# Performance work log

Measured on AMD Instinct MI355X. Metric: run time of the kernel, lower is better.

The kernel has to match this reference:

```python
import jax, jax.numpy as jnp
import numpy as np

N_BOND = 2_000_000
N_ATOM = 100_000
N_STRUCT = 2
THREEBODY_CUTOFF = 0.8


def setup_inputs() -> dict:
    key = jax.random.key(0)
    k1, k2 = jax.random.split(key)
    # bonds grouped (sorted) by source atom, as _compute_threebody assumes
    bond_src = jnp.sort(jax.random.randint(k1, (N_BOND,), 0, N_ATOM))
    bond_length = jax.random.uniform(k2, (N_BOND,), dtype=jnp.float32)
    n_atoms = jnp.full((N_STRUCT,), N_ATOM // N_STRUCT, dtype=jnp.int32)
    return {"bond_src": bond_src, "bond_length": bond_length, "n_atoms": n_atoms}


def reference(bond_src, bond_length, n_atoms):
    """Vectorized equivalent of compute_threebody_indices.

    Returns (bond_indices [T,2] pairs of ORIGINAL bond ids, n_triple_ij [n_bond],
    n_triple_i [n_atom], n_triple_s [n_struct]). Replaces the O(n) Python loops
    with segment-sum (degree count), prefix-sum (CSR offsets) and a flat
    enumeration of ordered within-atom bond pairs (j != k).
    """
    n_bond = bond_src.shape[0]
    n_atom = int(jnp.sum(n_atoms))
    n_struct = n_atoms.shape[0]

    # --- filter bonds by three-body cutoff, remember original bond ids ---
    mask = bond_length <= THREEBODY_CUTOFF
    kept = jnp.nonzero(mask)[0]          # original bond indices of surviving bonds
    src = bond_src[kept]                 # still sorted (subset of a sorted array)

    # --- per-atom bond counts and CSR offsets (parallel histogram + scan) ---
    deg = jax.ops.segment_sum(jnp.ones_like(src), src, num_segments=n_atom)
    bond_offset = jnp.cumsum(deg) - deg  # start of each atom's bond block

    # --- triples per atom / per bond / per structure ---
    n_triple_i = deg * (deg - 1)
    T = int(jnp.sum(n_triple_i))

    # --- enumerate all ordered pairs (j, k), j != k, within each atom block ---
    tri_atom = jnp.repeat(jnp.arange(n_atom), n_triple_i, total_repeat_length=T)
    tri_start = (jnp.cumsum(n_triple_i) - n_triple_i)[tri_atom]
    t = jnp.arange(T) - tri_start        # local triple index in [0, d*(d-1))
    d = deg[tri_atom]                    # d >= 2 wherever triples exist
    j = t // (d - 1)
    kp = t % (d - 1)
    k = kp + (kp >= j).astype(kp.dtype)  # skip k == j, preserving loop order
    b0 = bond_offset[tri_atom] + j       # relative (filtered) bond index
    b1 = bond_offset[tri_atom] + k
    bond_indices = jnp.stack([kept[b0], kept[b1]], axis=1)  # back to ORIGINAL ids

    # angles per ORIGINAL bond: deg(src)-1 for surviving bonds, 0 for filtered
    n_triple_ij = jnp.zeros(n_bond, dtype=deg.dtype).at[kept].set(deg[src] - 1)

    # angles per structure
    struct_id = jnp.repeat(jnp.arange(n_struct), n_atoms, total_repeat_length=n_atom)
    n_triple_s = jax.ops.segment_sum(n_triple_i, struct_id, num_segments=n_struct)

    return bond_indices, n_triple_ij, n_triple_i, n_triple_s
```

## Files before the change

kernel.cpp:

```cpp
#include <hip/hip_runtime.h>


#define CUTOFF 0.8f
#define NATOM_C 100000
#define MAXD 256

__global__ void k0_init(int* wstart, int* wend, int* deg, int* done, int n_atom) {
    int i = blockIdx.x * blockDim.x + threadIdx.x;
    if (i < n_atom) { wstart[i] = 0; wend[i] = 0; deg[i] = 0; }
    if (i == 0) *done = 0;
}

__global__ void kA_bounds_deg(const int* __restrict__ src, const float* __restrict__ len,
                              int* __restrict__ wstart, int* __restrict__ wend,
                              int* __restrict__ deg, int n_bond) {
    int q  = blockIdx.x * blockDim.x + threadIdx.x;
    int g0 = q * 4;
    int lane = threadIdx.x & 63;
    bool full = (g0 + 3 < n_bond);

    int4   s4 = make_int4(-3, -3, -3, -3);
    float4 l4 = make_float4(1e9f, 1e9f, 1e9f, 1e9f);
    if (full) {
        s4 = *(const int4*)(src + g0);
        l4 = *(const float4*)(len + g0);
    }
    int prevN = __shfl_up(s4.w, 1);
    int nextN = __shfl_down(s4.x, 1);
    if (lane == 0)  prevN = (g0 > 0 && g0 - 1 < n_bond) ? src[g0 - 1] : -1;
    if (lane == 63) nextN = (g0 + 4 < n_bond) ? src[g0 + 4] : -2;
    if (g0 + 4 >= n_bond) nextN = -2;

    if (full) {
        int a0 = s4.x, a1 = s4.y, a2 = s4.z, a3 = s4.w;
        if (g0 == 0 || a0 != prevN) wstart[a0] = g0;
        if (a1 != a0) wstart[a1] = g0 + 1;
        if (a2 != a1) wstart[a2] = g0 + 2;
        if (a3 != a2) wstart[a3] = g0 + 3;
        if (a0 != a1) wend[a0] = g0 + 1;
        if (a1 != a2) wend[a1] = g0 + 2;
        if (a2 != a3) wend[a2] = g0 + 3;
        if (g0 + 4 == n_bond || a3 != nextN) wend[a3] = g0 + 4;
        int c0 = (l4.x <= CUTOFF) ? 1 : 0;
        int c1 = (l4.y <= CUTOFF) ? 1 : 0;
        int c2 = (l4.z <= CUTOFF) ? 1 : 0;
        int c3 = (l4.w <= CUTOFF) ? 1 : 0;
        int aCur = a0, cnt = c0;
        if (a1 != aCur) { if (cnt) atomicAdd(&deg[aCur], cnt); aCur = a1; cnt = 0; }
        cnt += c1;
        if (a2 != aCur) { if (cnt) atomicAdd(&deg[aCur], cnt); aCur = a2; cnt = 0; }
        cnt += c2;
        if (a3 != aCur) { if (cnt) atomicAdd(&deg[aCur], cnt); aCur = a3; cnt = 0; }
        cnt += c3;
        if (cnt) atomicAdd(&deg[aCur], cnt);
    } else if (g0 < n_bond) {
        for (int j = 0; j < 4; j++) {
            int g = g0 + j;
            if (g >= n_bond) break;
            int a = src[g];
            if (g == 0 || src[g - 1] != a) wstart[a] = g;
            if (g == n_bond - 1 || src[g + 1] != a) wend[a] = g + 1;
            if (len[g] <= CUTOFF) atomicAdd(&deg[a], 1);
        }
    }
}

__global__ void kBC_scan(const int* __restrict__ deg, int* __restrict__ out_i,
                         int* __restrict__ exsc, int* __restrict__ bsums,
                         int* __restrict__ done, const int* __restrict__ n_atoms_arr,
                         int* __restrict__ out_s,
                         int n_atom, int ntiles, int n_struct) {
    __shared__ int tmp[256];
    __shared__ int isLast;
    int t = threadIdx.x;
    int base = blockIdx.x * 1024 + t * 4;
    int v0 = 0, v1 = 0, v2 = 0, v3 = 0;
    if (base + 3 < n_atom) {
        int4 d4 = *(const int4*)(deg + base);
        v0 = d4.x * (d4.x - 1); v1 = d4.y * (d4.y - 1);
        v2 = d4.z * (d4.z - 1); v3 = d4.w * (d4.w - 1);
        *(int4*)(out_i + base) = make_int4(v0, v1, v2, v3);
    } else {
        if (base     < n_atom) { int d = deg[base];     v0 = d * (d - 1); out_i[base]     = v0; }
        if (base + 1 < n_atom) { int d = deg[base + 1]; v1 = d * (d - 1); out_i[base + 1] = v1; }
        if (base + 2 < n_atom) { int d = deg[base + 2]; v2 = d * (d - 1); out_i[base + 2] = v2; }
        if (base + 3 < n_atom) { int d = deg[base + 3]; v3 = d * (d - 1); out_i[base + 3] = v3; }
    }
    int s = v0 + v1 + v2 + v3;
    tmp[t] = s;
    __syncthreads();
    for (int off = 1; off < 256; off <<= 1) {
        int v = (t >= off) ? tmp[t - off] : 0;
        __syncthreads();
        tmp[t] += v;
        __syncthreads();
    }
    int excl = tmp[t] - s;
    if (base     < n_atom) exsc[base]     = excl;
    if (base + 1 < n_atom) exsc[base + 1] = excl + v0;
    if (base + 2 < n_atom) exsc[base + 2] = excl + v0 + v1;
    if (base + 3 < n_atom) exsc[base + 3] = excl + v0 + v1 + v2;
    if (t == 255) bsums[blockIdx.x] = tmp[255];
    __syncthreads();
    if (t == 0) {
        __threadfence();
        int old = __hip_atomic_fetch_add(done, 1, __ATOMIC_ACQ_REL,
                                         __HIP_MEMORY_SCOPE_AGENT);
        isLast = (old == (int)gridDim.x - 1);
    }
    __syncthreads();
    if (!isLast) return;

    int v = 0;
    if (t < ntiles)
        v = __hip_atomic_load(&bsums[t], __ATOMIC_RELAXED, __HIP_MEMORY_SCOPE_AGENT);
    tmp[t] = v;
    __syncthreads();
    for (int off = 1; off < 256; off <<= 1) {
        int x = (t >= off) ? tmp[t - off] : 0;
        __syncthreads();
        tmp[t] += x;
        __syncthreads();
    }
    if (t < ntiles) bsums[t] = tmp[t] - v;
    int total = tmp[255];
    __threadfence_block();
    __syncthreads();
    if (t == 0) {
        int off = 0, prevA = 0;
        for (int s2 = 0; s2 < n_struct; s2++) {
            off += n_atoms_arr[s2];
            int A;
            if (off >= n_atom) A = total;
            else A = __hip_atomic_load(&exsc[off], __ATOMIC_RELAXED,
                                       __HIP_MEMORY_SCOPE_AGENT) + bsums[off >> 10];
            out_s[s2] = A - prevA;
            prevA = A;
        }
    }
}

__global__ void kD_enum(const float* __restrict__ len, const int* __restrict__ wstart,
                        const int* __restrict__ wend, const int* __restrict__ exsc,
                        const int* __restrict__ bsums,
                        int4* __restrict__ out4, int* __restrict__ out_ij,
                        int n_atom) {
    __shared__ int keptIds[4 * MAXD];
    int wave = threadIdx.x >> 6;
    int lane = threadIdx.x & 63;
    int a = blockIdx.x * 4 + wave;
    int* my = &keptIds[wave * MAXD];
    if (a >= n_atom) return;
    int s = wstart[a], e = wend[a];
    int d = 0;
    for (int base = s; base < e; base += 64) {
        int idx = base + lane;
        bool m = (idx < e) && (len[idx] <= CUTOFF);
        unsigned long long bal = __ballot(m);
        int pos = d + __popcll(bal & ((1ull << lane) - 1ull));
        if (m && pos < MAXD) my[pos] = idx;
        d += __popcll(bal);
    }
    int dm1 = d - 1;
    for (int idx = s + lane; idx < e; idx += 64)
        out_ij[idx] = (len[idx] <= CUTOFF) ? dm1 : 0;
    if (d >= 2) {
        unsigned udm1 = (unsigned)dm1;
        unsigned nP = ((unsigned)(d * dm1)) >> 1;
        int b4 = (exsc[a] + bsums[a >> 10]) >> 1;
        for (unsigned p = lane; p < nP; p += 64) {
            unsigned t0 = 2u * p;
            unsigned j  = t0 / udm1;
            unsigned kp = t0 - j * udm1;
            unsigned j1 = j, kp1 = kp + 1;
            if (kp1 == udm1) { j1++; kp1 = 0; }
            unsigned k0 = kp  + (kp  >= j  ? 1u : 0u);
            unsigned k1 = kp1 + (kp1 >= j1 ? 1u : 0u);
            out4[b4 + p] = make_int4(my[j], my[k0], my[j1], my[k1]);
        }
    }
}

extern "C" void kernel_launch(void* const* d_in, const int* in_sizes, int n_in,
                              void* d_out, int out_size, void* d_ws, size_t ws_size,
                              hipStream_t stream) {
    const int*   bond_src    = (const int*)d_in[0];
    const float* bond_len    = (const float*)d_in[1];
    const int*   n_atoms_arr = (const int*)d_in[2];
    int n_bond   = in_sizes[0];
    int n_struct = in_sizes[2];
    const int n_atom = NATOM_C;
    int T2 = out_size - n_bond - n_atom - n_struct;

    int ntiles = (n_atom + 1023) / 1024;

    int* ws     = (int*)d_ws;
    int* wstart = ws;
    int* wend   = ws + n_atom;
    int* deg    = ws + 2 * n_atom;
    int* exsc   = ws + 3 * n_atom;
    int* bsums  = exsc + n_atom;
    int* done   = bsums + ntiles;

    int*  out       = (int*)d_out;
    int4* out_pairs = (int4*)out;
    int*  out_ij    = out + T2;
    int*  out_i     = out_ij + n_bond;
    int*  out_s     = out_i + n_atom;

    int nq = (n_bond + 3) / 4;

    k0_init      <<<(n_atom + 255) / 256, 256, 0, stream>>>(wstart, wend, deg, done, n_atom);
    kA_bounds_deg<<<(nq + 255) / 256, 256, 0, stream>>>(bond_src, bond_len, wstart, wend, deg, n_bond);
    kBC_scan     <<<ntiles, 256, 0, stream>>>(deg, out_i, exsc, bsums, done, n_atoms_arr,
                                              out_s, n_atom, ntiles, n_struct);
    kD_enum      <<<(n_atom + 3) / 4, 256, 0, stream>>>(bond_len, wstart, wend, exsc, bsums,
                                                        out_pairs, out_ij, n_atom);
}
```

Baseline: 256.6 us.

## Fold init into bounds kernel and replace degree atomics with wave ballot counts

Drops the separate zero-init kernel: head threads now zero the entries for atoms with no bonds lying between consecutive sources, and the last thread clears the trailing atoms. Degree counting switches from per-atom atomicAdd to ballot/popcount over runs within a wave, with a serial backward scan when a run crosses a wave boundary, and one thread per bond instead of four. kD_enum caches the ballot masks for the first 256 bonds so the out_ij write does not reload lengths. This removes a launch and the atomics, at the cost of scalar loads and serial fallback loops for long or gapped runs.

```diff
diff --git a/kernel.cpp b/kernel.cpp
--- a/kernel.cpp
+++ b/kernel.cpp
@@ -5,63 +5,54 @@
 #define NATOM_C 100000
 #define MAXD 256
 
-__global__ void k0_init(int* wstart, int* wend, int* deg, int* done, int n_atom) {
-    int i = blockIdx.x * blockDim.x + threadIdx.x;
-    if (i < n_atom) { wstart[i] = 0; wend[i] = 0; deg[i] = 0; }
-    if (i == 0) *done = 0;
-}
-
 __global__ void kA_bounds_deg(const int* __restrict__ src, const float* __restrict__ len,
                               int* __restrict__ wstart, int* __restrict__ wend,
-                              int* __restrict__ deg, int n_bond) {
-    int q  = blockIdx.x * blockDim.x + threadIdx.x;
-    int g0 = q * 4;
+                              int* __restrict__ deg, int* __restrict__ done,
+                              int n_bond, int n_atom) {
+    int i = blockIdx.x * blockDim.x + threadIdx.x;
+    if (i == 0) *done = 0;
     int lane = threadIdx.x & 63;
-    bool full = (g0 + 3 < n_bond);
-
-    int4   s4 = make_int4(-3, -3, -3, -3);
-    float4 l4 = make_float4(1e9f, 1e9f, 1e9f, 1e9f);
-    if (full) {
-        s4 = *(const int4*)(src + g0);
-        l4 = *(const float4*)(len + g0);
-    }
-    int prevN = __shfl_up(s4.w, 1);
-    int nextN = __shfl_down(s4.x, 1);
-    if (lane == 0)  prevN = (g0 > 0 && g0 - 1 < n_bond) ? src[g0 - 1] : -1;
-    if (lane == 63) nextN = (g0 + 4 < n_bond) ? src[g0 + 4] : -2;
-    if (g0 + 4 >= n_bond) nextN = -2;
-
-    if (full) {
-        int a0 = s4.x, a1 = s4.y, a2 = s4.z, a3 = s4.w;
-        if (g0 == 0 || a0 != prevN) wstart[a0] = g0;
-        if (a1 != a0) wstart[a1] = g0 + 1;
-        if (a2 != a1) wstart[a2] = g0 + 2;
-        if (a3 != a2) wstart[a3] = g0 + 3;
-        if (a0 != a1) wend[a0] = g0 + 1;
-        if (a1 != a2) wend[a1] = g0 + 2;
-        if (a2 != a3) wend[a2] = g0 + 3;
-        if (g0 + 4 == n_bond || a3 != nextN) wend[a3] = g0 + 4;
-        int c0 = (l4.x <= CUTOFF) ? 1 : 0;
-        int c1 = (l4.y <= CUTOFF) ? 1 : 0;
-        int c2 = (l4.z <= CUTOFF) ? 1 : 0;
-        int c3 = (l4.w <= CUTOFF) ? 1 : 0;
-        int aCur = a0, cnt = c0;
-        if (a1 != aCur) { if (cnt) atomicAdd(&deg[aCur], cnt); aCur = a1; cnt = 0; }
-        cnt += c1;
-        if (a2 != aCur) { if (cnt) atomicAdd(&deg[aCur], cnt); aCur = a2; cnt = 0; }
-        cnt += c2;
-        if (a3 != aCur) { if (cnt) atomicAdd(&deg[aCur], cnt); aCur = a3; cnt = 0; }
-        cnt += c3;
-        if (cnt) atomicAdd(&deg[aCur], cnt);
-    } else if (g0 < n_bond) {
-        for (int j = 0; j < 4; j++) {
-            int g = g0 + j;
-            if (g >= n_bond) break;
-            int a = src[g];
-            if (g == 0 || src[g - 1] != a) wstart[a] = g;
-            if (g == n_bond - 1 || src[g + 1] != a) wend[a] = g + 1;
-            if (len[g] <= CUTOFF) atomicAdd(&deg[a], 1);
-        }
+    bool valid = i < n_bond;
+    int a = -1; bool kept = false;
+    if (valid) { a = src[i]; kept = (len[i] <= CUTOFF); }
+
+    int ap = __shfl_up(a, 1);
+    if (lane == 0) ap = (valid && i > 0) ? src[i - 1] : -1;
+    int an = __shfl_down(a, 1);
+    if (lane == 63) an = (valid && i + 1 < n_bond) ? src[i + 1] : -2;
+
+    bool head = valid && (i == 0 || ap != a);
+    bool tail = valid && (i == n_bond - 1 || an != a);
+
+    unsigned long long keptB = __ballot(kept);
+    unsigned long long headB = __ballot(head);
+
+    if (head) {
+        wstart[a] = i;
+        int p = (i == 0) ? -1 : ap;
+        for (int g = p + 1; g < a; ++g) { wstart[g] = 0; wend[g] = 0; deg[g] = 0; }
+    }
+    if (tail) {
+        wend[a] = i + 1;
+        if (i == n_bond - 1)
+            for (int g = a + 1; g < n_atom; ++g) { wstart[g] = 0; wend[g] = 0; deg[g] = 0; }
+
+        unsigned long long belowInc = (lane == 63) ? ~0ull : ((2ull << lane) - 1ull);
+        unsigned long long h = headB & belowInc;
+        int cnt;
+        if (h) {
+            int runStartLane = 63 - __clzll(h);
+            unsigned long long runMask = belowInc & ~((1ull << runStartLane) - 1ull);
+            cnt = __popcll(keptB & runMask);
+        } else {
+            cnt = __popcll(keptB & belowInc);
+            int wbase = i - lane;
+            for (int j = wbase - 1; j >= 0; --j) {
+                if (src[j] != a) break;
+                if (len[j] <= CUTOFF) cnt++;
+            }
+        }
+        deg[a] = cnt;
     }
 }
 
@@ -153,17 +144,38 @@
     if (a >= n_atom) return;
     int s = wstart[a], e = wend[a];
     int d = 0;
-    for (int base = s; base < e; base += 64) {
+    unsigned long long bal[4] = {0ull, 0ull, 0ull, 0ull};
+#pragma unroll
+    for (int it = 0; it < 4; ++it) {
+        int base = s + it * 64;
+        if (base < e) {
+            int idx = base + lane;
+            bool m = (idx < e) && (len[idx] <= CUTOFF);
+            unsigned long long b = __ballot(m);
+            bal[it] = b;
+            int pos = d + __popcll(b & ((1ull << lane) - 1ull));
+            if (m && pos < MAXD) my[pos] = idx;
+            d += __popcll(b);
+        }
+    }
+    for (int base = s + 256; base < e; base += 64) {
         int idx = base + lane;
         bool m = (idx < e) && (len[idx] <= CUTOFF);
-        unsigned long long bal = __ballot(m);
-        int pos = d + __popcll(bal & ((1ull << lane) - 1ull));
+        unsigned long long b = __ballot(m);
+        int pos = d + __popcll(b & ((1ull << lane) - 1ull));
         if (m && pos < MAXD) my[pos] = idx;
-        d += __popcll(bal);
+        d += __popcll(b);
     }
     int dm1 = d - 1;
-    for (int idx = s + lane; idx < e; idx += 64)
-        out_ij[idx] = (len[idx] <= CUTOFF) ? dm1 : 0;
+#pragma unroll
+    for (int it = 0; it < 4; ++it) {
+        int idx = s + it * 64 + lane;
+        if (idx < e) out_ij[idx] = ((bal[it] >> lane) & 1ull) ? dm1 : 0;
+    }
+    for (int base = s + 256; base < e; base += 64) {
+        int idx = base + lane;
+        if (idx < e) out_ij[idx] = (len[idx] <= CUTOFF) ? dm1 : 0;
+    }
     if (d >= 2) {
         unsigned udm1 = (unsigned)dm1;
         unsigned nP = ((unsigned)(d * dm1)) >> 1;
@@ -208,10 +220,8 @@
     int*  out_i     = out_ij + n_bond;
     int*  out_s     = out_i + n_atom;
 
-    int nq = (n_bond + 3) / 4;
-
-    k0_init      <<<(n_atom + 255) / 256, 256, 0, stream>>>(wstart, wend, deg, done, n_atom);
-    kA_bounds_deg<<<(nq + 255) / 256, 256, 0, stream>>>(bond_src, bond_len, wstart, wend, deg, n_bond);
+    kA_bounds_deg<<<(n_bond + 255) / 256, 256, 0, stream>>>(bond_src, bond_len, wstart, wend,
+                                                            deg, done, n_bond, n_atom);
     kBC_scan     <<<ntiles, 256, 0, stream>>>(deg, out_i, exsc, bsums, done, n_atoms_arr,
                                               out_s, n_atom, ntiles, n_struct);
     kD_enum      <<<(n_atom + 3) / 4, 256, 0, stream>>>(bond_len, wstart, wend, exsc, bsums,
```

Result: no change. 259.9 us (+1.3%).
